# Optimization experiments

Hardware: AMD Instinct MI355X
Metric: run time of the kernel (lower is better)

Reference implementation:

```python
import jax, jax.numpy as jnp
import numpy as np

BS, N, D_ENT, K, D_IN, D_F, H, L, S = 128, 512, 256, 128, 1024, 256, 128, 2, 64
MAX_ENTITY_NUM = 512.0
TEMP = 1.0
NEG = -1e9


def _ln(x, g, b, eps=1e-5):
    m = jnp.mean(x, -1, keepdims=True)
    v = jnp.mean((x - m) ** 2, -1, keepdims=True)
    return (x - m) * jax.lax.rsqrt(v + eps) * g + b


def setup_inputs() -> dict:
    key = jax.random.key(0)
    ks = jax.random.split(key, 16)
    nrm = lambda k, sh, s=0.02: jax.random.normal(k, sh, jnp.float32) * s
    entity_num = jax.random.randint(ks[0], (BS,), 64, N)
    selected_units = jax.random.randint(ks[1], (BS, S), 0, N + 1) % (entity_num[:, None] + 1)
    selected_units_num = jax.random.randint(ks[2], (BS,), 1, S + 1).at[0].set(S)  # max == S so torch seq_len == S
    return dict(
        embedding=nrm(ks[3], (BS, D_IN), 1.0),
        entity_embedding=nrm(ks[4], (BS, N, D_ENT), 1.0),
        key_w=nrm(ks[5], (K, D_ENT)), key_b=jnp.zeros((K,), jnp.float32),
        q1_w=nrm(ks[6], (D_F, D_IN)), q1_b=jnp.zeros((D_F,), jnp.float32),
        q2_w=nrm(ks[7], (K, D_F)), q2_b=jnp.zeros((K,), jnp.float32),
        e1_w=nrm(ks[8], (D_F, K)), e1_b=jnp.zeros((D_F,), jnp.float32),
        e2_w=nrm(ks[9], (D_IN, D_F)), e2_b=jnp.zeros((D_IN,), jnp.float32),
        end_embedding=nrm(ks[10], (1, K), 0.09),
        lstm_wih=nrm(ks[11], (L, 4 * H, K)),
        lstm_whh=nrm(ks[12], (L, 4 * H, H)),
        ln_ig=jnp.ones((L, 4 * H), jnp.float32), ln_ib=jnp.zeros((L, 4 * H), jnp.float32),
        ln_hg=jnp.ones((L, 4 * H), jnp.float32), ln_hb=jnp.zeros((L, 4 * H), jnp.float32),
        ln_cg=jnp.ones((L, H), jnp.float32), ln_cb=jnp.zeros((L, H), jnp.float32),
        entity_num=entity_num, selected_units=selected_units, selected_units_num=selected_units_num,
    )


def _forward(embedding, entity_embedding, key_w, key_b, q1_w, q1_b, q2_w, q2_b,
             e1_w, e1_b, e2_w, e2_b, end_embedding, lstm_wih, lstm_whh,
             ln_ig, ln_ib, ln_hg, ln_hb, ln_cg, ln_cb,
             entity_num, selected_units, selected_units_num):
    bs = embedding.shape[0]
    ar = jnp.arange(bs)
    # keys: [bs, N+1, K] with end-embedding placed at position entity_num
    key = jnp.einsum('bnd,kd->bnk', entity_embedding, key_w) + key_b
    key = jnp.concatenate([key, jnp.zeros((bs, 1, K), key.dtype)], axis=1)
    key = key.at[ar, entity_num].set(end_embedding[0])
    # entity_reduce_type == 'constant': key_embeddings = embed_mlp(key / MAX_ENTITY_NUM)
    kr = key / MAX_ENTITY_NUM
    key_emb = jax.nn.relu(jnp.einsum('bnk,fk->bnf', kr, e1_w) + e1_b)
    key_emb = jnp.einsum('bnf,df->bnd', key_emb, e2_w) + e2_b  # [bs, N+1, D_IN]
    # precompute per-step masks (cumulative disabling of previously selected units;
    # end token blocked only at step 0, then re-enabled unless selected)
    init_mask = jnp.arange(N + 1)[None, :] < (entity_num + 1)[:, None]
    oh = jax.nn.one_hot(selected_units, N + 1, dtype=jnp.int32)
    prev = jnp.cumsum(oh, axis=1) - oh  # selected strictly before step i
    mask_seq = init_mask[:, None, :] & (prev == 0)  # [bs, S, N+1]
    mask_seq = mask_seq.at[ar, 0, entity_num].set(False)

    def step(carry, xs):
        ae, hs, cs = carry
        i, su_i, m_i = xs
        # query MLP
        x = jax.nn.relu(ae @ q1_w.T + q1_b) @ q2_w.T + q2_b  # [bs, K]
        new_hs, new_cs = [], []
        for l in range(L):  # layer-norm LSTM stack
            gates = _ln(x @ lstm_wih[l].T, ln_ig[l], ln_ib[l]) + _ln(hs[l] @ lstm_whh[l].T, ln_hg[l], ln_hb[l])
            ig, fg, gg, og = jnp.split(gates, 4, axis=-1)
            c = _ln(jax.nn.sigmoid(fg) * cs[l] + jax.nn.sigmoid(ig) * jnp.tanh(gg), ln_cg[l], ln_cb[l])
            h = jax.nn.sigmoid(og) * jnp.tanh(c)
            new_hs.append(h); new_cs.append(c)
            x = h
        logits = jnp.where(m_i, jnp.einsum('bk,bnk->bn', x, key) / TEMP, NEG)
        gate = ((i + 1) <= selected_units_num) & (su_i != entity_num)
        ae = ae + key_emb[ar, su_i] * gate[:, None].astype(ae.dtype)
        return (ae, jnp.stack(new_hs), jnp.stack(new_cs)), logits

    hs0 = jnp.zeros((L, bs, H), embedding.dtype)
    cs0 = jnp.zeros((L, bs, H), embedding.dtype)
    (ae, _, _), logits = jax.lax.scan(
        step, (embedding, hs0, cs0),
        (jnp.arange(S), selected_units.T, jnp.swapaxes(mask_seq, 0, 1)))
    return jnp.swapaxes(logits, 0, 1), ae  # logits [bs, S, N+1]


def reference(embedding, entity_embedding, key_w, key_b, q1_w, q1_b, q2_w, q2_b,
              e1_w, e1_b, e2_w, e2_b, end_embedding, lstm_wih, lstm_whh,
              ln_ig, ln_ib, ln_hg, ln_hb, ln_cg, ln_cb,
              entity_num, selected_units, selected_units_num):
    logits, ae = _forward(embedding, entity_embedding, key_w, key_b, q1_w, q1_b, q2_w, q2_b,
                          e1_w, e1_b, e2_w, e2_b, end_embedding, lstm_wih, lstm_whh,
                          ln_ig, ln_ib, ln_hg, ln_hb, ln_cg, ln_cb,
                          entity_num, selected_units, selected_units_num)
    # torch forward returns (logits, units=None, embedding, selected_units_num); units omitted here
    return logits, ae, selected_units_num
```

## Files before the change

### kernel.cpp

```cpp
#include <hip/hip_runtime.h>
#include <hip/hip_bf16.h>
#include <math.h>

#define BSZ   128
#define NENT  512
#define NP1   513
#define DENT  256
#define KDIM  128
#define DIN   1024
#define DF    256
#define HDIM  128
#define SSTEP 64
#define G4    512
#define NEGV  (-1e9f)
#define INV_MAX (1.0f/512.0f)

typedef float v2f __attribute__((ext_vector_type(2)));
typedef __attribute__((ext_vector_type(8))) short bf16x8;
typedef __attribute__((ext_vector_type(4))) float f32x4;
typedef long i64;

__device__ inline float sigf(float x){ return 1.f/(1.f+__expf(-x)); }
__device__ inline float tanh_fast(float x){ float e=__expf(2.f*x); return 1.f - 2.f/(e+1.f); }

__device__ inline float sum16_partial(float x){
  x += __int_as_float(__builtin_amdgcn_update_dpp(0, __float_as_int(x), 0x111, 0xf, 0xf, true));
  x += __int_as_float(__builtin_amdgcn_update_dpp(0, __float_as_int(x), 0x112, 0xf, 0xf, true));
  x += __int_as_float(__builtin_amdgcn_update_dpp(0, __float_as_int(x), 0x114, 0xf, 0xf, true));
  x += __int_as_float(__builtin_amdgcn_update_dpp(0, __float_as_int(x), 0x118, 0xf, 0xf, true));
  return x;
}
__device__ inline float wave_sum_partial(float x){
  x = sum16_partial(x);
  x += __int_as_float(__builtin_amdgcn_update_dpp(0, __float_as_int(x), 0x142, 0xa, 0xf, true));
  x += __int_as_float(__builtin_amdgcn_update_dpp(0, __float_as_int(x), 0x143, 0xc, 0xf, true));
  return x;
}
__device__ inline float wave_sum(float x){
  return __int_as_float(__builtin_amdgcn_readlane(__float_as_int(wave_sum_partial(x)), 63));
}

__device__ inline unsigned pk8(float4 f){
  int r = 0;
  r = __builtin_amdgcn_cvt_pk_fp8_f32(f.x, f.y, r, false);
  r = __builtin_amdgcn_cvt_pk_fp8_f32(f.z, f.w, r, true);
  return (unsigned)r;
}
__device__ inline i64 u2l(uint2 v){ union{uint2 u; i64 l;} x; x.u=v; return x.l; }

__device__ inline float2 block_reduce2(float x, float y, float* red){
  float sx0 = wave_sum_partial(x), sy0 = wave_sum_partial(y);
  int w = threadIdx.x>>6;
  __syncthreads();
  if((threadIdx.x&63)==63){ red[w]=sx0; red[8+w]=sy0; }
  __syncthreads();
  float sx=0.f, sy=0.f;
  #pragma unroll
  for(int q=0;q<8;q++){ sx+=red[q]; sy+=red[8+q]; }
  return make_float2(sx,sy);
}

template<bool BKMAJOR, bool RELU, bool GATHER>
__global__ __launch_bounds__(256)
void mfma_gemm(const float* __restrict__ A, const float* __restrict__ B,
               const float* __restrict__ bias, float* __restrict__ C,
               int M, int N, int K,
               const int* __restrict__ gidx, float scale){
  __shared__ ushort Abf[64][72];
  __shared__ ushort Bbf[64][72];
  const int t = threadIdx.x;
  const int bm = blockIdx.x, bn = blockIdx.y;
  const int w = t>>6, l = t&63;
  const int lm = l&15, lg = l>>4;
  const int r0 = w*16;
  f32x4 acc[4];
  #pragma unroll
  for(int f=0;f<4;f++) acc[f] = (f32x4){0.f,0.f,0.f,0.f};

  for(int k0=0;k0<K;k0+=64){
    #pragma unroll
    for(int i=0;i<4;i++){
      int idx = t + i*256;
      int row = idx>>4, c4 = (idx&15)<<2;
      const float* src;
      if(GATHER){
        int gr = bm*64+row;
        src = &A[((size_t)(gr>>6)*NP1 + gidx[gr])*(size_t)K + k0 + c4];
      } else {
        src = &A[((size_t)bm*64+row)*K + k0 + c4];
      }
      float4 v = *(const float4*)src;
      if(GATHER){ v.x*=scale; v.y*=scale; v.z*=scale; v.w*=scale; }
      ushort4 u;
      u.x = __float_as_uint(v.x)>>16; u.y = __float_as_uint(v.y)>>16;
      u.z = __float_as_uint(v.z)>>16; u.w = __float_as_uint(v.w)>>16;
      *(ushort4*)&Abf[row][c4] = u;
    }
    if(!BKMAJOR){
      #pragma unroll
      for(int i=0;i<4;i++){
        int idx = t + i*256;
        int row = idx>>4, c4 = (idx&15)<<2;
        float4 v = *(const float4*)&B[((size_t)bn*64+row)*K + k0 + c4];
        ushort4 u;
        u.x = __float_as_uint(v.x)>>16; u.y = __float_as_uint(v.y)>>16;
        u.z = __float_as_uint(v.z)>>16; u.w = __float_as_uint(v.w)>>16;
        *(ushort4*)&Bbf[row][c4] = u;
      }
    } else {
      #pragma unroll
      for(int i=0;i<4;i++){
        int idx = t + i*256;
        int kr = idx>>4, n4 = (idx&15)<<2;
        float4 v = *(const float4*)&B[(size_t)(k0+kr)*N + bn*64 + n4];
        Bbf[n4+0][kr] = __float_as_uint(v.x)>>16;
        Bbf[n4+1][kr] = __float_as_uint(v.y)>>16;
        Bbf[n4+2][kr] = __float_as_uint(v.z)>>16;
        Bbf[n4+3][kr] = __float_as_uint(v.w)>>16;
      }
    }
    __syncthreads();
    #pragma unroll
    for(int kk=0;kk<64;kk+=32){
      bf16x8 a = *(const bf16x8*)&Abf[r0+lm][kk + lg*8];
      #pragma unroll
      for(int f=0;f<4;f++){
        bf16x8 b = *(const bf16x8*)&Bbf[f*16+lm][kk + lg*8];
        acc[f] = __builtin_amdgcn_mfma_f32_16x16x32_bf16(a, b, acc[f], 0,0,0);
      }
    }
    __syncthreads();
  }
  #pragma unroll
  for(int f=0;f<4;f++){
    int gcol = bn*64 + f*16 + lm;
    float bb = bias ? bias[gcol] : 0.f;
    #pragma unroll
    for(int r=0;r<4;r++){
      int grow = bm*64 + r0 + lg*4 + r;
      float v = acc[f][r] + bb;
      if(RELU) v = fmaxf(v, 0.f);
      C[(size_t)grow*N + gcol] = v;
    }
  }
}

__global__ __launch_bounds__(256)
void key_gemm_mfma(const float* __restrict__ A, const float* __restrict__ W,
                   const float* __restrict__ bias, const int* __restrict__ en,
                   const float* __restrict__ end_emb, float* __restrict__ C){
  __shared__ ushort Abf[64][264];
  __shared__ ushort Bbf[128][264];
  __shared__ float bs[128];
  const int t = threadIdx.x;
  const int bm = blockIdx.x;
  #pragma unroll
  for(int i=0;i<16;i++){
    int idx = t + i*256;
    int row = idx>>6, c4 = (idx&63)<<2;
    float4 v = *(const float4*)&A[((size_t)bm*64+row)*256 + c4];
    ushort4 u;
    u.x = __float_as_uint(v.x)>>16; u.y = __float_as_uint(v.y)>>16;
    u.z = __float_as_uint(v.z)>>16; u.w = __float_as_uint(v.w)>>16;
    *(ushort4*)&Abf[row][c4] = u;
  }
  #pragma unroll
  for(int i=0;i<32;i++){
    int idx = t + i*256;
    int row = idx>>6, c4 = (idx&63)<<2;
    float4 v = *(const float4*)&W[(size_t)row*256 + c4];
    ushort4 u;
    u.x = __float_as_uint(v.x)>>16; u.y = __float_as_uint(v.y)>>16;
    u.z = __float_as_uint(v.z)>>16; u.w = __float_as_uint(v.w)>>16;
    *(ushort4*)&Bbf[row][c4] = u;
  }
  if(t<128) bs[t] = bias[t];
  __syncthreads();
  const int w = t>>6, l = t&63;
  const int lm = l&15, lg = l>>4;
  const int r0 = w*16;
  f32x4 acc[8];
  #pragma unroll
  for(int f=0;f<8;f++) acc[f] = (f32x4){0.f,0.f,0.f,0.f};
  #pragma unroll
  for(int k0=0;k0<256;k0+=32){
    bf16x8 a = *(const bf16x8*)&Abf[r0+lm][k0 + lg*8];
    #pragma unroll
    for(int f=0;f<8;f++){
      bf16x8 b = *(const bf16x8*)&Bbf[f*16+lm][k0 + lg*8];
      acc[f] = __builtin_amdgcn_mfma_f32_16x16x32_bf16(a, b, acc[f], 0,0,0);
    }
  }
  #pragma unroll
  for(int f=0;f<8;f++){
    int gcol = f*16 + lm;
    float bb = bs[gcol];
    float ev = end_emb[gcol];
    #pragma unroll
    for(int r=0;r<4;r++){
      int grow = bm*64 + r0 + lg*4 + r;
      int bq = grow>>9, n = grow&511;
      size_t orow = (size_t)bq*NP1 + n;
      float v = acc[f][r] + bb;
      if(n == en[bq]) v = ev;
      C[orow*KDIM + gcol] = v;
    }
  }
}

__global__ __launch_bounds__(256)
void g0_gemm_ln(const float* __restrict__ X, const float* __restrict__ W,
                const float* __restrict__ gam, const float* __restrict__ bet,
                float* __restrict__ G0){
  __shared__ ushort Abf[16][136];
  __shared__ float redS[16][4], redQ[16][4];
  const int t = threadIdx.x, bm = blockIdx.x;
  const int w = t>>6, l = t&63, lm = l&15, lg = l>>4;
  {
    int idx = t*8;
    int row = idx>>7, c = idx&127;
    const float* src = &X[((size_t)bm*16+row)*128 + c];
    float4 a = *(const float4*)src;
    float4 d = *(const float4*)(src+4);
    ushort4 u0, u1;
    u0.x=__float_as_uint(a.x)>>16; u0.y=__float_as_uint(a.y)>>16;
    u0.z=__float_as_uint(a.z)>>16; u0.w=__float_as_uint(a.w)>>16;
    u1.x=__float_as_uint(d.x)>>16; u1.y=__float_as_uint(d.y)>>16;
    u1.z=__float_as_uint(d.z)>>16; u1.w=__float_as_uint(d.w)>>16;
    *(ushort4*)&Abf[row][c] = u0;
    *(ushort4*)&Abf[row][c+4] = u1;
  }
  __syncthreads();
  f32x4 acc[8];
  #pragma unroll
  for(int f=0;f<8;f++) acc[f] = (f32x4){0.f,0.f,0.f,0.f};
  #pragma unroll
  for(int kt=0;kt<4;kt++){
    int k0 = kt*32;
    bf16x8 a = *(const bf16x8*)&Abf[lm][k0 + lg*8];
    #pragma unroll
    for(int f=0;f<8;f++){
      int brow = w*128 + f*16 + lm;
      const float* bp = &W[(size_t)brow*128 + k0 + lg*8];
      float4 b0 = *(const float4*)bp;
      float4 b1 = *(const float4*)(bp+4);
      bf16x8 bfr;
      bfr[0]=(short)(__float_as_uint(b0.x)>>16); bfr[1]=(short)(__float_as_uint(b0.y)>>16);
      bfr[2]=(short)(__float_as_uint(b0.z)>>16); bfr[3]=(short)(__float_as_uint(b0.w)>>16);
      bfr[4]=(short)(__float_as_uint(b1.x)>>16); bfr[5]=(short)(__float_as_uint(b1.y)>>16);
      bfr[6]=(short)(__float_as_uint(b1.z)>>16); bfr[7]=(short)(__float_as_uint(b1.w)>>16);
      acc[f] = __builtin_amdgcn_mfma_f32_16x16x32_bf16(a, bfr, acc[f], 0,0,0);
    }
  }
  float mu[4], rs[4];
  #pragma unroll
  for(int r=0;r<4;r++){
    float s=0.f, q=0.f;
    #pragma unroll
    for(int f=0;f<8;f++){ float x=acc[f][r]; s+=x; q+=x*x; }
    s = sum16_partial(s);
    q = sum16_partial(q);
    if(lm==15){ redS[lg*4+r][w]=s; redQ[lg*4+r][w]=q; }
  }
  __syncthreads();
  #pragma unroll
  for(int r=0;r<4;r++){
    int row = lg*4+r;
    float S = redS[row][0]+redS[row][1]+redS[row][2]+redS[row][3];
    float Q = redQ[row][0]+redQ[row][1]+redQ[row][2]+redQ[row][3];
    mu[r] = S*(1.f/512.f);
    rs[r] = rsqrtf(Q*(1.f/512.f) - mu[r]*mu[r] + 1e-5f);
  }
  #pragma unroll
  for(int f=0;f<8;f++){
    int col = w*128 + f*16 + lm;
    float g = gam[col], bt = bet[col];
    #pragma unroll
    for(int r=0;r<4;r++){
      int grow = bm*16 + lg*4 + r;
      G0[(size_t)grow*G4 + col] = (acc[f][r]-mu[r])*rs[r]*g + bt;
    }
  }
}

__global__ __launch_bounds__(256)
void c0_kernel(const float* __restrict__ q1_w, const float* __restrict__ e2_b,
               float* __restrict__ c0v){
  __shared__ float red[4];
  int f = blockIdx.x, t = threadIdx.x;
  float4 a = *(const float4*)&q1_w[(size_t)f*DIN + t*4];
  float4 e = *(const float4*)&e2_b[t*4];
  float p = a.x*e.x + a.y*e.y + a.z*e.z + a.w*e.w;
  float s = wave_sum_partial(p);
  if((t&63)==63) red[t>>6] = s;
  __syncthreads();
  if(t==0) c0v[f] = red[0]+red[1]+red[2]+red[3];
}

__global__ void prefix_kernel(const float* __restrict__ U0, const float* __restrict__ Q1K,
                              const float* __restrict__ c0v, const float* __restrict__ T1,
                              const int* __restrict__ su, const int* __restrict__ en,
                              const int* __restrict__ sun,
                              float* __restrict__ RU, float* __restrict__ s1,
                              float* __restrict__ ngout){
  int b = blockIdx.x, f = threadIdx.x;
  float acc = U0[b*DF+f];
  float c0f = c0v[f];
  float s1a = 0.f, ng = 0.f;
  int enb = en[b], sunb = sun[b];
  for(int j=0;j<SSTEP;j++){
    int r = b*SSTEP+j;
    float q = Q1K[(size_t)r*DF+f];
    float tt = T1[(size_t)r*DF+f];
    RU[(size_t)r*DF+f] = fmaxf(acc,0.f);
    int sj = su[r];
    float g = ((j+1)<=sunb && sj!=enb) ? 1.f : 0.f;
    acc = fmaf(g, q + c0f, acc);
    s1a = fmaf(g, tt, s1a);
    ng += g;
  }
  s1[b*DF+f]=s1a;
  if(f==0) ngout[b]=ng;
}

__global__ __launch_bounds__(512)
__attribute__((amdgpu_waves_per_eu(2,2)))
void lstm_serial(const float* __restrict__ wih, const float* __restrict__ whh,
                 const float* __restrict__ G0,
                 const float* __restrict__ ln_ig, const float* __restrict__ ln_ib,
                 const float* __restrict__ ln_hg, const float* __restrict__ ln_hb,
                 const float* __restrict__ ln_cg, const float* __restrict__ ln_cb,
                 float* __restrict__ H1){
  const int b = blockIdx.x;
  const int j = threadIdx.x;
  const int w = j>>6, l = j&63;
  const int lm = l&15, lg = l>>4;
  __shared__ uint2 W0f[4][4][512];
  __shared__ uint2 W1f[4][4][512];
  __shared__ uint4 h0q8[8], h1q8[8];
  __shared__ float pvv[512], pv1[512];
  __shared__ float lnA[512], lnB[512], lnC[512], lnD[512], lnE[512], lnF[512];
  __shared__ float red[32];

  {
    unsigned dw[32];
    #pragma unroll
    for(int q=0;q<32;q++) dw[q] = pk8(*(const float4*)&whh[(size_t)j*KDIM + q*4]);
    #pragma unroll
    for(int kt=0;kt<4;kt++)
      #pragma unroll
      for(int g=0;g<4;g++)
        W0f[kt][g][j] = make_uint2(dw[kt*8+g*2], dw[kt*8+g*2+1]);
    #pragma unroll
    for(int q=0;q<32;q++) dw[q] = pk8(*(const float4*)&wih[65536 + (size_t)j*KDIM + q*4]);
    #pragma unroll
    for(int kt=0;kt<4;kt++)
      #pragma unroll
      for(int g=0;g<4;g++)
        W1f[kt][g][j] = make_uint2(dw[kt*8+g*2], dw[kt*8+g*2+1]);
  }
  uint2 w2f[4][4];
  #pragma unroll
  for(int c=0;c<4;c++){
    int row = w*64 + c*16 + lm;
    #pragma unroll
    for(int kt=0;kt<4;kt++){
      int k0 = kt*32 + lg*8;
      float4 x0 = *(const float4*)&whh[65536 + (size_t)row*KDIM + k0];
      float4 x1 = *(const float4*)&whh[65536 + (size_t)row*KDIM + k0 + 4];
      w2f[c][kt] = make_uint2(pk8(x0), pk8(x1));
    }
  }
  lnA[j] = ln_hg[j];     lnB[j] = ln_hb[j];
  lnC[j] = ln_ig[512+j]; lnD[j] = ln_ib[512+j];
  lnE[j] = ln_hg[512+j]; lnF[j] = ln_hb[512+j];

  float cg0A=0.f,cb0A=0.f,cg0B=0.f,cb0B=0.f;
  float cg1A=0.f,cb1A=0.f,cg1B=0.f,cb1B=0.f;
  float c0rA=0.f,c0rB=0.f,c1rA=0.f,c1rB=0.f;
  if(j<64){
    cg0A=ln_cg[j];      cb0A=ln_cb[j];
    cg0B=ln_cg[j+64];   cb0B=ln_cb[j+64];
    cg1A=ln_cg[128+j];    cb1A=ln_cb[128+j];
    cg1B=ln_cg[128+j+64]; cb1B=ln_cb[128+j+64];
  }
  if(j<8){ h0q8[j]=(uint4){0,0,0,0}; h1q8[j]=(uint4){0,0,0,0}; }
  __syncthreads();

  const int colbase = w*64;

  for(int i=0;i<SSTEP;i++){
    float g0a[4], g0b[4];
    if(j<64){
      const float* gp = &G0[((size_t)b*SSTEP+i)*G4];
      #pragma unroll
      for(int k=0;k<4;k++){ g0a[k]=gp[j+128*k]; g0b[k]=gp[j+64+128*k]; }
    }

    f32x4 accv[4], acc1[4];
    #pragma unroll
    for(int c=0;c<4;c++){ accv[c]=(f32x4){0.f,0.f,0.f,0.f}; acc1[c]=(f32x4){0.f,0.f,0.f,0.f}; }
    #pragma unroll
    for(int kt=0;kt<4;kt++){
      uint2 a0 = make_uint2(0,0), a1 = make_uint2(0,0);
      if(lm==0){
        a0 = *(const uint2*)((const char*)h0q8 + kt*32 + lg*8);
        a1 = *(const uint2*)((const char*)h1q8 + kt*32 + lg*8);
      }
      i64 A0 = u2l(a0), A1 = u2l(a1);
      #pragma unroll
      for(int c=0;c<4;c++){
        accv[c] = __builtin_amdgcn_mfma_f32_16x16x32_fp8_fp8(A0, u2l(W0f[kt][lg][colbase+c*16+lm]), accv[c], 0,0,0);
        acc1[c] = __builtin_amdgcn_mfma_f32_16x16x32_fp8_fp8(A1, u2l(w2f[c][kt]), acc1[c], 0,0,0);
      }
    }
    {
      float sv=0.f, sq=0.f, s1v=0.f, s1q=0.f;
      #pragma unroll
      for(int c=0;c<4;c++){
        float x = accv[c][0]; sv += x; sq += x*x;
        float y = acc1[c][0]; s1v += y; s1q += y*y;
      }
      float a  = wave_sum_partial(sv);
      float bq = wave_sum_partial(sq);
      float c2 = wave_sum_partial(s1v);
      float d  = wave_sum_partial(s1q);
      if(l==63){ red[w]=a; red[8+w]=bq; red[16+w]=c2; red[24+w]=d; }
      if(l<16){
        #pragma unroll
        for(int c=0;c<4;c++){
          pvv[colbase + c*16 + l] = accv[c][0];
          pv1[colbase + c*16 + l] = acc1[c][0];
        }
      }
    }
    __syncthreads();

    if(j<64){
      float S=0.f,S2=0.f;
      #pragma unroll
      for(int q=0;q<8;q++){ S+=red[q]; S2+=red[8+q]; }
      float mu = S*(1.f/512.f);
      float rs = rsqrtf(S2*(1.f/512.f) - mu*mu + 1e-5f);
      float ashA[4], ashB[4];
      #pragma unroll
      for(int k=0;k<4;k++){
        int ia = j + 128*k, ib = j + 64 + 128*k;
        ashA[k] = g0a[k] + (pvv[ia]-mu)*rs*lnA[ia] + lnB[ia];
        ashB[k] = g0b[k] + (pvv[ib]-mu)*rs*lnA[ib] + lnB[ib];
      }
      float cpA = sigf(ashA[1])*c0rA + sigf(ashA[0])*tanh_fast(ashA[2]);
      float cpB = sigf(ashB[1])*c0rB + sigf(ashB[0])*tanh_fast(ashB[2]);
      float s  = wave_sum(cpA+cpB);
      float s2 = wave_sum(cpA*cpA+cpB*cpB);
      float muc = s*(1.f/128.f);
      float rsc = rsqrtf(s2*(1.f/128.f) - muc*muc + 1e-5f);
      c0rA = (cpA-muc)*rsc*cg0A + cb0A;
      c0rB = (cpB-muc)*rsc*cg0B + cb0B;
      float hA = sigf(ashA[3])*tanh_fast(c0rA);
      float hB = sigf(ashB[3])*tanh_fast(c0rB);
      ((unsigned char*)h0q8)[j]    = (unsigned char)(__builtin_amdgcn_cvt_pk_fp8_f32(hA,hA,0,false)&0xff);
      ((unsigned char*)h0q8)[j+64] = (unsigned char)(__builtin_amdgcn_cvt_pk_fp8_f32(hB,hB,0,false)&0xff);
    }
    __syncthreads();

    f32x4 accu[4];
    #pragma unroll
    for(int c=0;c<4;c++) accu[c]=(f32x4){0.f,0.f,0.f,0.f};
    #pragma unroll
    for(int kt=0;kt<4;kt++){
      uint2 a0 = make_uint2(0,0);
      if(lm==0) a0 = *(const uint2*)((const char*)h0q8 + kt*32 + lg*8);
      i64 A0 = u2l(a0);
      #pragma unroll
      for(int c=0;c<4;c++){
        accu[c] = __builtin_amdgcn_mfma_f32_16x16x32_fp8_fp8(A0, u2l(W1f[kt][lg][colbase+c*16+lm]), accu[c], 0,0,0);
      }
    }
    {
      float su=0.f, squ=0.f;
      #pragma unroll
      for(int c=0;c<4;c++){ float x=accu[c][0]; su+=x; squ+=x*x; }
      float a  = wave_sum_partial(su);
      float bq = wave_sum_partial(squ);
      if(l==63){ red[w]=a; red[8+w]=bq; }
      if(l<16){
        #pragma unroll
        for(int c=0;c<4;c++) pvv[colbase + c*16 + l] = accu[c][0];
      }
    }
    __syncthreads();

    if(j<64){
      float Su=0.f,Su2=0.f,Sv=0.f,Sv2=0.f;
      #pragma unroll
      for(int q=0;q<8;q++){ Su+=red[q]; Su2+=red[8+q]; Sv+=red[16+q]; Sv2+=red[24+q]; }
      float muu = Su*(1.f/512.f);
      float rsu = rsqrtf(Su2*(1.f/512.f) - muu*muu + 1e-5f);
      float muv = Sv*(1.f/512.f);
      float rsv = rsqrtf(Sv2*(1.f/512.f) - muv*muv + 1e-5f);
      float ashA[4], ashB[4];
      #pragma unroll
      for(int k=0;k<4;k++){
        int ia = j + 128*k, ib = j + 64 + 128*k;
        ashA[k] = (pvv[ia]-muu)*rsu*lnC[ia] + lnD[ia]
                + (pv1[ia]-muv)*rsv*lnE[ia] + lnF[ia];
        ashB[k] = (pvv[ib]-muu)*rsu*lnC[ib] + lnD[ib]
                + (pv1[ib]-muv)*rsv*lnE[ib] + lnF[ib];
      }
      float cpA = sigf(ashA[1])*c1rA + sigf(ashA[0])*tanh_fast(ashA[2]);
      float cpB = sigf(ashB[1])*c1rB + sigf(ashB[0])*tanh_fast(ashB[2]);
      float s  = wave_sum(cpA+cpB);
      float s2 = wave_sum(cpA*cpA+cpB*cpB);
      float muc = s*(1.f/128.f);
      float rsc = rsqrtf(s2*(1.f/128.f) - muc*muc + 1e-5f);
      c1rA = (cpA-muc)*rsc*cg1A + cb1A;
      c1rB = (cpB-muc)*rsc*cg1B + cb1B;
      float hA = sigf(ashA[3])*tanh_fast(c1rA);
      float hB = sigf(ashB[3])*tanh_fast(c1rB);
      ((unsigned char*)h1q8)[j]    = (unsigned char)(__builtin_amdgcn_cvt_pk_fp8_f32(hA,hA,0,false)&0xff);
      ((unsigned char*)h1q8)[j+64] = (unsigned char)(__builtin_amdgcn_cvt_pk_fp8_f32(hB,hB,0,false)&0xff);
      H1[((size_t)b*SSTEP+i)*HDIM + j]      = hA;
      H1[((size_t)b*SSTEP+i)*HDIM + j + 64] = hB;
    }
    __syncthreads();
  }
}

__global__ __launch_bounds__(512)
void logits_kernel(const float* __restrict__ key, const float* __restrict__ H1,
                   const int* __restrict__ en, const int* __restrict__ su,
                   float* __restrict__ out){
  const int b = blockIdx.x;
  const int ihalf = blockIdx.y;
  __shared__ float HsT[128][36];
  __shared__ int firstsel[NP1];
  for(int t=threadIdx.x; t<32*HDIM; t+=512){
    int il = t>>7, k = t&127;
    HsT[k][il] = H1[(size_t)b*SSTEP*HDIM + (size_t)(ihalf*32+il)*HDIM + k];
  }
  for(int t=threadIdx.x; t<NP1; t+=512) firstsel[t] = 1<<30;
  __syncthreads();
  if(threadIdx.x < SSTEP) atomicMin(&firstsel[su[b*SSTEP+threadIdx.x]], (int)threadIdx.x);
  __syncthreads();
  const int enb = en[b];
  const int tn = threadIdx.x & 255;
  const int ig = threadIdx.x >> 8;
  const int i0l = ig*16;
  const int ig0 = ihalf*32 + i0l;
  float acc0[16], acc1[16];
  #pragma unroll
  for(int q=0;q<16;q++){ acc0[q]=0.f; acc1[q]=0.f; }
  const float* kr0 = key + ((size_t)b*NP1 + tn)*KDIM;
  const float* kr1 = key + ((size_t)b*NP1 + tn + 256)*KDIM;
  for(int k=0;k<KDIM;k+=4){
    float4 kv0 = *(const float4*)&kr0[k];
    float4 kv1 = *(const float4*)&kr1[k];
    float k0a[4] = {kv0.x,kv0.y,kv0.z,kv0.w};
    float k1a[4] = {kv1.x,kv1.y,kv1.z,kv1.w};
    #pragma unroll
    for(int kk=0;kk<4;kk++){
      float4 h0 = *(const float4*)&HsT[k+kk][i0l+0];
      float4 h1 = *(const float4*)&HsT[k+kk][i0l+4];
      float4 h2 = *(const float4*)&HsT[k+kk][i0l+8];
      float4 h3 = *(const float4*)&HsT[k+kk][i0l+12];
      float ka = k0a[kk], kb = k1a[kk];
      acc0[ 0]=fmaf(ka,h0.x,acc0[ 0]); acc0[ 1]=fmaf(ka,h0.y,acc0[ 1]);
      acc0[ 2]=fmaf(ka,h0.z,acc0[ 2]); acc0[ 3]=fmaf(ka,h0.w,acc0[ 3]);
      acc0[ 4]=fmaf(ka,h1.x,acc0[ 4]); acc0[ 5]=fmaf(ka,h1.y,acc0[ 5]);
      acc0[ 6]=fmaf(ka,h1.z,acc0[ 6]); acc0[ 7]=fmaf(ka,h1.w,acc0[ 7]);
      acc0[ 8]=fmaf(ka,h2.x,acc0[ 8]); acc0[ 9]=fmaf(ka,h2.y,acc0[ 9]);
      acc0[10]=fmaf(ka,h2.z,acc0[10]); acc0[11]=fmaf(ka,h2.w,acc0[11]);
      acc0[12]=fmaf(ka,h3.x,acc0[12]); acc0[13]=fmaf(ka,h3.y,acc0[13]);
      acc0[14]=fmaf(ka,h3.z,acc0[14]); acc0[15]=fmaf(ka,h3.w,acc0[15]);
      acc1[ 0]=fmaf(kb,h0.x,acc1[ 0]); acc1[ 1]=fmaf(kb,h0.y,acc1[ 1]);
      acc1[ 2]=fmaf(kb,h0.z,acc1[ 2]); acc1[ 3]=fmaf(kb,h0.w,acc1[ 3]);
      acc1[ 4]=fmaf(kb,h1.x,acc1[ 4]); acc1[ 5]=fmaf(kb,h1.y,acc1[ 5]);
      acc1[ 6]=fmaf(kb,h1.z,acc1[ 6]); acc1[ 7]=fmaf(kb,h1.w,acc1[ 7]);
      acc1[ 8]=fmaf(kb,h2.x,acc1[ 8]); acc1[ 9]=fmaf(kb,h2.y,acc1[ 9]);
      acc1[10]=fmaf(kb,h2.z,acc1[10]); acc1[11]=fmaf(kb,h2.w,acc1[11]);
      acc1[12]=fmaf(kb,h3.x,acc1[12]); acc1[13]=fmaf(kb,h3.y,acc1[13]);
      acc1[14]=fmaf(kb,h3.z,acc1[14]); acc1[15]=fmaf(kb,h3.w,acc1[15]);
    }
  }
  const int n0 = tn, n1 = tn + 256;
  const int fs0 = firstsel[n0], fs1 = firstsel[n1];
  #pragma unroll
  for(int q=0;q<16;q++){
    int i = ig0 + q;
    bool m0 = (n0 <= enb) && (fs0 >= i) && !(i==0 && n0==enb);
    bool m1 = (n1 <= enb) && (fs1 >= i) && !(i==0 && n1==enb);
    out[((size_t)b*SSTEP + i)*NP1 + n0] = m0 ? acc0[q] : NEGV;
    out[((size_t)b*SSTEP + i)*NP1 + n1] = m1 ? acc1[q] : NEGV;
  }
  if(threadIdx.x < 32){
    int i = ihalf*32 + threadIdx.x;
    out[((size_t)b*SSTEP + i)*NP1 + 512] = NEGV;
  }
}

__global__ __launch_bounds__(256)
void ae_gemm(const float* __restrict__ A, const float* __restrict__ B,
             const float* __restrict__ emb, const float* __restrict__ e2_b,
             const float* __restrict__ ng, const int* __restrict__ sun,
             float* __restrict__ out){
  const size_t AE_OFF = (size_t)BSZ*SSTEP*NP1;
  const size_t SUN_OFF = AE_OFF + (size_t)BSZ*DIN;
  __shared__ ushort Abf[64][72];
  __shared__ ushort Bbf[64][72];
  const int t = threadIdx.x;
  const int bm = blockIdx.x, bn = blockIdx.y;
  const int w = t>>6, l = t&63;
  const int lm = l&15, lg = l>>4;
  const int r0 = w*16;
  f32x4 acc[4];
  #pragma unroll
  for(int f=0;f<4;f++) acc[f] = (f32x4){0.f,0.f,0.f,0.f};
  for(int k0=0;k0<256;k0+=64){
    #pragma unroll
    for(int i=0;i<4;i++){
      int idx = t + i*256;
      int row = idx>>4, c4 = (idx&15)<<2;
      float4 v = *(const float4*)&A[((size_t)bm*64+row)*256 + k0 + c4];
      ushort4 u;
      u.x = __float_as_uint(v.x)>>16; u.y = __float_as_uint(v.y)>>16;
      u.z = __float_as_uint(v.z)>>16; u.w = __float_as_uint(v.w)>>16;
      *(ushort4*)&Abf[row][c4] = u;
    }
    #pragma unroll
    for(int i=0;i<4;i++){
      int idx = t + i*256;
      int row = idx>>4, c4 = (idx&15)<<2;
      float4 v = *(const float4*)&B[((size_t)bn*64+row)*256 + k0 + c4];
      ushort4 u;
      u.x = __float_as_uint(v.x)>>16; u.y = __float_as_uint(v.y)>>16;
      u.z = __float_as_uint(v.z)>>16; u.w = __float_as_uint(v.w)>>16;
      *(ushort4*)&Bbf[row][c4] = u;
    }
    __syncthreads();
    #pragma unroll
    for(int kk=0;kk<64;kk+=32){
      bf16x8 a = *(const bf16x8*)&Abf[r0+lm][kk + lg*8];
      #pragma unroll
      for(int f=0;f<4;f++){
        bf16x8 b = *(const bf16x8*)&Bbf[f*16+lm][kk + lg*8];
        acc[f] = __builtin_amdgcn_mfma_f32_16x16x32_bf16(a, b, acc[f], 0,0,0);
      }
    }
    __syncthreads();
  }
  #pragma unroll
  for(int f=0;f<4;f++){
    int gcol = bn*64 + f*16 + lm;
    float eb = e2_b[gcol];
    #pragma unroll
    for(int r=0;r<4;r++){
      int grow = bm*64 + r0 + lg*4 + r;
      size_t o = (size_t)grow*DIN + gcol;
      out[AE_OFF + o] = emb[o] + acc[f][r] + ng[grow]*eb;
    }
  }
  if(bm==0 && bn==0 && t<BSZ) out[SUN_OFF + t] = (float)sun[t];
}

extern "C" void kernel_launch(void* const* d_in, const int* in_sizes, int n_in,
                              void* d_out, int out_size, void* d_ws, size_t ws_size,
                              hipStream_t stream){
  const float* emb     = (const float*)d_in[0];
  const float* ent     = (const float*)d_in[1];
  const float* key_w   = (const float*)d_in[2];
  const float* key_b   = (const float*)d_in[3];
  const float* q1_w    = (const float*)d_in[4];
  const float* q1_b    = (const float*)d_in[5];
  const float* q2_w    = (const float*)d_in[6];
  const float* q2_b    = (const float*)d_in[7];
  const float* e1_w    = (const float*)d_in[8];
  const float* e1_b    = (const float*)d_in[9];
  const float* e2_w    = (const float*)d_in[10];
  const float* e2_b    = (const float*)d_in[11];
  const float* end_emb = (const float*)d_in[12];
  const float* wih     = (const float*)d_in[13];
  const float* whh     = (const float*)d_in[14];
  const float* ln_ig   = (const float*)d_in[15];
  const float* ln_ib   = (const float*)d_in[16];
  const float* ln_hg   = (const float*)d_in[17];
  const float* ln_hb   = (const float*)d_in[18];
  const float* ln_cg   = (const float*)d_in[19];
  const float* ln_cb   = (const float*)d_in[20];
  const int* en  = (const int*)d_in[21];
  const int* su  = (const int*)d_in[22];
  const int* sun = (const int*)d_in[23];
  float* out = (float*)d_out;
  float* ws  = (float*)d_ws;

  const size_t o_key = 0;
  const size_t o_T1  = o_key + 8404992;
  const size_t o_q1e = o_T1  + 2097152;
  const size_t o_c0  = o_q1e + 65536;
  const size_t o_U0  = o_c0  + 1024;
  const size_t o_Q1K = o_U0  + 32768;
  const size_t o_RU  = o_Q1K + 2097152;
  const size_t o_X   = o_RU  + 2097152;
  const size_t o_G0  = o_X   + 1048576;
  const size_t o_s1  = o_G0  + 4194304;
  const size_t o_ng  = o_s1  + 32768;
  const size_t o_H1  = o_ng  + 1024;

  key_gemm_mfma<<<1024,256,0,stream>>>(ent, key_w, key_b, en, end_emb, ws+o_key);
  mfma_gemm<false,true,true><<<dim3(128,4),256,0,stream>>>(ws+o_key, e1_w, e1_b, ws+o_T1,
                                                           8192,256,128, su, INV_MAX);
  mfma_gemm<true,false,false><<<dim3(4,4),256,0,stream>>>(q1_w, e2_w, nullptr, ws+o_q1e,
                                                          256,256,1024, nullptr, 1.f);
  c0_kernel<<<256,256,0,stream>>>(q1_w, e2_b, ws+o_c0);
  mfma_gemm<false,false,false><<<dim3(2,4),256,0,stream>>>(emb, q1_w, q1_b, ws+o_U0,
                                                           128,256,1024, nullptr, 1.f);
  mfma_gemm<false,false,false><<<dim3(128,4),256,0,stream>>>(ws+o_T1, ws+o_q1e, nullptr, ws+o_Q1K,
                                                             8192,256,256, nullptr, 1.f);
  prefix_kernel<<<128,256,0,stream>>>(ws+o_U0, ws+o_Q1K, ws+o_c0, ws+o_T1, su, en, sun,
                                      ws+o_RU, ws+o_s1, ws+o_ng);
  mfma_gemm<false,false,false><<<dim3(128,2),256,0,stream>>>(ws+o_RU, q2_w, q2_b, ws+o_X,
                                                             8192,128,256, nullptr, 1.f);
  g0_gemm_ln<<<512,256,0,stream>>>(ws+o_X, wih, ln_ig, ln_ib, ws+o_G0);
  lstm_serial<<<128,512,0,stream>>>(wih, whh, ws+o_G0,
                                    ln_ig, ln_ib, ln_hg, ln_hb, ln_cg, ln_cb, ws+o_H1);
  logits_kernel<<<dim3(128,2),512,0,stream>>>(ws+o_key, ws+o_H1, en, su, out);
  ae_gemm<<<dim3(2,16),256,0,stream>>>(ws+o_s1, e2_w, emb, e2_b, ws+o_ng, sun, out);
}
```

Before: 440.3 us.

## Replicate LSTM cell update across all waves to cut block barriers per step

```diff
diff --git a/kernel.cpp b/kernel.cpp
--- a/kernel.cpp
+++ b/kernel.cpp
@@ -337,10 +337,10 @@
   const int lm = l&15, lg = l>>4;
   __shared__ uint2 W0f[4][4][512];
   __shared__ uint2 W1f[4][4][512];
-  __shared__ uint4 h0q8[8], h1q8[8];
-  __shared__ float pvv[512], pv1[512];
+  __shared__ uint4 h0own[8][8], h1own[8][8];
+  __shared__ float pvv[2][512], pv1[2][512], pu[2][512];
   __shared__ float lnA[512], lnB[512], lnC[512], lnD[512], lnE[512], lnF[512];
-  __shared__ float red[32];
+  __shared__ float red[2][48];
 
   {
     unsigned dw[32];
@@ -375,26 +375,23 @@
   lnC[j] = ln_ig[512+j]; lnD[j] = ln_ib[512+j];
   lnE[j] = ln_hg[512+j]; lnF[j] = ln_hb[512+j];
 
-  float cg0A=0.f,cb0A=0.f,cg0B=0.f,cb0B=0.f;
-  float cg1A=0.f,cb1A=0.f,cg1B=0.f,cb1B=0.f;
+  float cg0A=ln_cg[l],     cb0A=ln_cb[l];
+  float cg0B=ln_cg[l+64],  cb0B=ln_cb[l+64];
+  float cg1A=ln_cg[128+l],    cb1A=ln_cb[128+l];
+  float cg1B=ln_cg[128+l+64], cb1B=ln_cb[128+l+64];
   float c0rA=0.f,c0rB=0.f,c1rA=0.f,c1rB=0.f;
-  if(j<64){
-    cg0A=ln_cg[j];      cb0A=ln_cb[j];
-    cg0B=ln_cg[j+64];   cb0B=ln_cb[j+64];
-    cg1A=ln_cg[128+j];    cb1A=ln_cb[128+j];
-    cg1B=ln_cg[128+j+64]; cb1B=ln_cb[128+j+64];
-  }
-  if(j<8){ h0q8[j]=(uint4){0,0,0,0}; h1q8[j]=(uint4){0,0,0,0}; }
+  if(l<8){ h0own[w][l]=(uint4){0,0,0,0}; h1own[w][l]=(uint4){0,0,0,0}; }
   __syncthreads();
 
   const int colbase = w*64;
+  int p = 0;
 
   for(int i=0;i<SSTEP;i++){
     float g0a[4], g0b[4];
-    if(j<64){
+    {
       const float* gp = &G0[((size_t)b*SSTEP+i)*G4];
       #pragma unroll
-      for(int k=0;k<4;k++){ g0a[k]=gp[j+128*k]; g0b[k]=gp[j+64+128*k]; }
+      for(int k=0;k<4;k++){ g0a[k]=gp[l+128*k]; g0b[k]=gp[l+64+128*k]; }
     }
 
     f32x4 accv[4], acc1[4];
@@ -404,8 +401,8 @@
     for(int kt=0;kt<4;kt++){
       uint2 a0 = make_uint2(0,0), a1 = make_uint2(0,0);
       if(lm==0){
-        a0 = *(const uint2*)((const char*)h0q8 + kt*32 + lg*8);
-        a1 = *(const uint2*)((const char*)h1q8 + kt*32 + lg*8);
+        a0 = *(const uint2*)((const char*)&h0own[w][0] + kt*32 + lg*8);
+        a1 = *(const uint2*)((const char*)&h1own[w][0] + kt*32 + lg*8);
       }
       i64 A0 = u2l(a0), A1 = u2l(a1);
       #pragma unroll
@@ -425,29 +422,29 @@
       float bq = wave_sum_partial(sq);
       float c2 = wave_sum_partial(s1v);
       float d  = wave_sum_partial(s1q);
-      if(l==63){ red[w]=a; red[8+w]=bq; red[16+w]=c2; red[24+w]=d; }
+      if(l==63){ red[p][w]=a; red[p][8+w]=bq; red[p][16+w]=c2; red[p][24+w]=d; }
       if(l<16){
         #pragma unroll
         for(int c=0;c<4;c++){
-          pvv[colbase + c*16 + l] = accv[c][0];
-          pv1[colbase + c*16 + l] = acc1[c][0];
+          pvv[p][colbase + c*16 + l] = accv[c][0];
+          pv1[p][colbase + c*16 + l] = acc1[c][0];
         }
       }
     }
     __syncthreads();
 
-    if(j<64){
+    {
       float S=0.f,S2=0.f;
       #pragma unroll
-      for(int q=0;q<8;q++){ S+=red[q]; S2+=red[8+q]; }
+      for(int q=0;q<8;q++){ S+=red[p][q]; S2+=red[p][8+q]; }
       float mu = S*(1.f/512.f);
       float rs = rsqrtf(S2*(1.f/512.f) - mu*mu + 1e-5f);
       float ashA[4], ashB[4];
       #pragma unroll
       for(int k=0;k<4;k++){
-        int ia = j + 128*k, ib = j + 64 + 128*k;
-        ashA[k] = g0a[k] + (pvv[ia]-mu)*rs*lnA[ia] + lnB[ia];
-        ashB[k] = g0b[k] + (pvv[ib]-mu)*rs*lnA[ib] + lnB[ib];
+        int ia = l + 128*k, ib = l + 64 + 128*k;
+        ashA[k] = g0a[k] + (pvv[p][ia]-mu)*rs*lnA[ia] + lnB[ia];
+        ashB[k] = g0b[k] + (pvv[p][ib]-mu)*rs*lnA[ib] + lnB[ib];
       }
       float cpA = sigf(ashA[1])*c0rA + sigf(ashA[0])*tanh_fast(ashA[2]);
       float cpB = sigf(ashB[1])*c0rB + sigf(ashB[0])*tanh_fast(ashB[2]);
@@ -459,10 +456,9 @@
       c0rB = (cpB-muc)*rsc*cg0B + cb0B;
       float hA = sigf(ashA[3])*tanh_fast(c0rA);
       float hB = sigf(ashB[3])*tanh_fast(c0rB);
-      ((unsigned char*)h0q8)[j]    = (unsigned char)(__builtin_amdgcn_cvt_pk_fp8_f32(hA,hA,0,false)&0xff);
-      ((unsigned char*)h0q8)[j+64] = (unsigned char)(__builtin_amdgcn_cvt_pk_fp8_f32(hB,hB,0,false)&0xff);
-    }
-    __syncthreads();
+      ((unsigned char*)&h0own[w][0])[l]    = (unsigned char)(__builtin_amdgcn_cvt_pk_fp8_f32(hA,hA,0,false)&0xff);
+      ((unsigned char*)&h0own[w][0])[l+64] = (unsigned char)(__builtin_amdgcn_cvt_pk_fp8_f32(hB,hB,0,false)&0xff);
+    }
 
     f32x4 accu[4];
     #pragma unroll
@@ -470,7 +466,7 @@
     #pragma unroll
     for(int kt=0;kt<4;kt++){
       uint2 a0 = make_uint2(0,0);
-      if(lm==0) a0 = *(const uint2*)((const char*)h0q8 + kt*32 + lg*8);
+      if(lm==0) a0 = *(const uint2*)((const char*)&h0own[w][0] + kt*32 + lg*8);
       i64 A0 = u2l(a0);
       #pragma unroll
       for(int c=0;c<4;c++){
@@ -483,18 +479,18 @@
       for(int c=0;c<4;c++){ float x=accu[c][0]; su+=x; squ+=x*x; }
       float a  = wave_sum_partial(su);
       float bq = wave_sum_partial(squ);
-      if(l==63){ red[w]=a; red[8+w]=bq; }
+      if(l==63){ red[p][32+w]=a; red[p][40+w]=bq; }
       if(l<16){
         #pragma unroll
-        for(int c=0;c<4;c++) pvv[colbase + c*16 + l] = accu[c][0];
+        for(int c=0;c<4;c++) pu[p][colbase + c*16 + l] = accu[c][0];
       }
     }
     __syncthreads();
 
-    if(j<64){
+    {
       float Su=0.f,Su2=0.f,Sv=0.f,Sv2=0.f;
       #pragma unroll
-      for(int q=0;q<8;q++){ Su+=red[q]; Su2+=red[8+q]; Sv+=red[16+q]; Sv2+=red[24+q]; }
+      for(int q=0;q<8;q++){ Su+=red[p][32+q]; Su2+=red[p][40+q]; Sv+=red[p][16+q]; Sv2+=red[p][24+q]; }
       float muu = Su*(1.f/512.f);
       float rsu = rsqrtf(Su2*(1.f/512.f) - muu*muu + 1e-5f);
       float muv = Sv*(1.f/512.f);
@@ -502,11 +498,11 @@
       float ashA[4], ashB[4];
       #pragma unroll
       for(int k=0;k<4;k++){
-        int ia = j + 128*k, ib = j + 64 + 128*k;
-        ashA[k] = (pvv[ia]-muu)*rsu*lnC[ia] + lnD[ia]
-                + (pv1[ia]-muv)*rsv*lnE[ia] + lnF[ia];
-        ashB[k] = (pvv[ib]-muu)*rsu*lnC[ib] + lnD[ib]
-                + (pv1[ib]-muv)*rsv*lnE[ib] + lnF[ib];
+        int ia = l + 128*k, ib = l + 64 + 128*k;
+        ashA[k] = (pu[p][ia]-muu)*rsu*lnC[ia] + lnD[ia]
+                + (pv1[p][ia]-muv)*rsv*lnE[ia] + lnF[ia];
+        ashB[k] = (pu[p][ib]-muu)*rsu*lnC[ib] + lnD[ib]
+                + (pv1[p][ib]-muv)*rsv*lnE[ib] + lnF[ib];
       }
       float cpA = sigf(ashA[1])*c1rA + sigf(ashA[0])*tanh_fast(ashA[2]);
       float cpB = sigf(ashB[1])*c1rB + sigf(ashB[0])*tanh_fast(ashB[2]);
@@ -518,12 +514,14 @@
       c1rB = (cpB-muc)*rsc*cg1B + cb1B;
       float hA = sigf(ashA[3])*tanh_fast(c1rA);
       float hB = sigf(ashB[3])*tanh_fast(c1rB);
-      ((unsigned char*)h1q8)[j]    = (unsigned char)(__builtin_amdgcn_cvt_pk_fp8_f32(hA,hA,0,false)&0xff);
-      ((unsigned char*)h1q8)[j+64] = (unsigned char)(__builtin_amdgcn_cvt_pk_fp8_f32(hB,hB,0,false)&0xff);
-      H1[((size_t)b*SSTEP+i)*HDIM + j]      = hA;
-      H1[((size_t)b*SSTEP+i)*HDIM + j + 64] = hB;
-    }
-    __syncthreads();
+      ((unsigned char*)&h1own[w][0])[l]    = (unsigned char)(__builtin_amdgcn_cvt_pk_fp8_f32(hA,hA,0,false)&0xff);
+      ((unsigned char*)&h1own[w][0])[l+64] = (unsigned char)(__builtin_amdgcn_cvt_pk_fp8_f32(hB,hB,0,false)&0xff);
+      if(w==0){
+        H1[((size_t)b*SSTEP+i)*HDIM + l]      = hA;
+        H1[((size_t)b*SSTEP+i)*HDIM + l + 64] = hB;
+      }
+    }
+    p ^= 1;
   }
 }
 
```

Result: slower. 501.4 us (+13.9%).
